# Optimization experiments

Hardware: AMD Instinct MI355X
Metric: run time of the kernel (lower is better)

## Reference

```python
import jax, jax.numpy as jnp
import numpy as np
import math

# Model dims (see init_kwargs)
B_SZ, L, D_MODEL = 1, 2048, 512
H, G, P, N, R = 16, 4, 64, 32, 2
RATIO = H // G
CHUNK = 256
EPS = 1e-5
DIM_Z = H * P
DIM_X = H * P
DIM_B = G * N * R
DIM_C = G * N * R
D_PROJ = DIM_Z + DIM_X + DIM_B + DIM_C + G + G


def setup_inputs() -> dict:
    key = jax.random.key(0)
    ks = jax.random.split(key, 8)
    u = jax.random.normal(ks[0], (B_SZ, L, D_MODEL), jnp.float32)
    W_in = jax.random.normal(ks[1], (D_PROJ, D_MODEL), jnp.float32) * (1.0 / math.sqrt(D_MODEL))
    b_in = np.zeros(D_PROJ, np.float32)
    # dt bias init: inverse softplus of dt ~ LogUniform(dt_min, dt_max)
    dt0 = np.exp(np.random.RandomState(0).rand(G) * (math.log(0.1) - math.log(0.001)) + math.log(0.001))
    inv_dt = dt0 + np.log(-np.expm1(-dt0))
    s = DIM_Z + DIM_X + DIM_B + DIM_C
    b_in[s:s + G] = inv_dt
    b_in[s + G:] = -3.0  # lambda bias
    b_in = jnp.asarray(b_in)
    W_xup = jax.random.normal(ks[2], (P * R, P), jnp.float32) * (1.0 / math.sqrt(P * R))
    W_ydown = jax.random.normal(ks[3], (P, P * R), jnp.float32) * (1.0 / math.sqrt(P * R))
    A_log = jnp.log(jax.random.uniform(ks[4], (G,), jnp.float32, 1.0, 16.0))
    theta_log = jax.random.normal(ks[5], (G, N // 2), jnp.float32)
    D = jnp.ones((H,), jnp.float32)
    norm_B_w = jnp.ones((N * R,), jnp.float32)
    norm_C_w = jnp.ones((N * R,), jnp.float32)
    bias_B = jnp.ones((G, N, R), jnp.float32)
    bias_C = jnp.ones((G, N, R), jnp.float32)
    W_out = jax.random.normal(ks[6], (D_MODEL, H * P), jnp.float32) * (1.0 / math.sqrt(H * P))
    return dict(u=u, W_in=W_in, b_in=b_in, W_xup=W_xup, W_ydown=W_ydown,
                A_log=A_log, theta_log=theta_log, D=D,
                norm_B_w=norm_B_w, norm_C_w=norm_C_w,
                bias_B=bias_B, bias_C=bias_C, W_out=W_out)


def _rms(x, w):
    return x * jax.lax.rsqrt(jnp.mean(x * x, axis=-1, keepdims=True) + EPS) * w


def _rope(x, ang):
    # x: (B,L,H,N,R), ang: (B,L,H,N/2) -- rotate interleaved (real,imag) pairs along N
    sh = x.shape
    xr = x.reshape(sh[:-2] + (N // 2, 2, R))
    re, im = xr[..., 0, :], xr[..., 1, :]
    c = jnp.cos(ang)[..., None]
    s = jnp.sin(ang)[..., None]
    out = jnp.stack([re * c - im * s, re * s + im * c], axis=-2)
    return out.reshape(sh)


def _chunk_scan(u, dt, A, C, cs):
    # u: (B,L,H,N,P), dt: (B,L,H), A: (H,), C: (B,L,H,N,R). L % cs == 0.
    B, Ltot, Hh, Nn, Pp = u.shape
    Rr = C.shape[-1]
    nc = Ltot // cs
    la = (dt * A).reshape(B, nc, cs, Hh)                      # log decay per step
    uc = u.reshape(B, nc, cs, Hh, Nn, Pp)
    Cc = C.reshape(B, nc, cs, Hh, Nn, Rr)
    # intra-chunk pairwise decay matrix (stable segsum)
    lap = la.transpose(0, 1, 3, 2)                            # (B,nc,H,cs)
    cums = jnp.cumsum(lap, axis=-1)
    seg = cums[..., :, None] - cums[..., None, :]
    mask = jnp.tril(jnp.ones((cs, cs), bool))
    Lmask = jnp.where(mask, jnp.exp(seg), 0.0)                # (B,nc,H,cs,cs)
    h_intra = jnp.einsum('bchij,bcjhnp->bcihnp', Lmask, uc)   # (B,nc,cs,H,N,P)
    y_diag = jnp.einsum('bclhnp,bclhnr->bclhpr', h_intra, Cc)
    decay_chunk = jnp.exp(jnp.sum(la, axis=2))                # (B,nc,H)
    h_last = h_intra[:, :, -1]                                # (B,nc,H,N,P)
    # inter-chunk sequential scan (state at the START of each chunk)
    def step(h, inp):
        d, cl = inp
        return h * d[:, :, None, None] + cl, h
    h0 = jnp.zeros((B, Hh, Nn, Pp), u.dtype)
    hF, h_states = jax.lax.scan(step, h0, (decay_chunk.transpose(1, 0, 2), h_last.transpose(1, 0, 2, 3, 4)))
    h_states = h_states.transpose(1, 0, 2, 3, 4)              # (B,nc,H,N,P)
    decay_intra = jnp.exp(jnp.cumsum(la, axis=2))             # (B,nc,cs,H)
    h_eff = jnp.einsum('bchnp,bclh->bclhnp', h_states, decay_intra)
    y_off = jnp.einsum('bclhnp,bclhnr->bclhpr', h_eff, Cc)
    y = (y_diag + y_off).reshape(B, Ltot, Hh, Pp, Rr)
    return y, hF


def reference(u, W_in, b_in, W_xup, W_ydown, A_log, theta_log, D,
              norm_B_w, norm_C_w, bias_B, bias_C, W_out):
    B_sz = u.shape[0]
    proj = u @ W_in.T + b_in                                  # (B,L,D_PROJ)
    s0, s1, s2, s3, s4 = DIM_Z, DIM_Z + DIM_X, DIM_Z + DIM_X + DIM_B, DIM_Z + DIM_X + DIM_B + DIM_C, DIM_Z + DIM_X + DIM_B + DIM_C + G
    z = proj[..., :s0]
    xp = proj[..., s0:s1].reshape(B_sz, L, H, P)
    Bp = proj[..., s1:s2]
    Cp = proj[..., s2:s3]
    dt = proj[..., s3:s4]                                     # (B,L,G)
    lam = proj[..., s4:]                                      # (B,L,G)
    xp = jax.nn.silu(xp)
    dt = jax.nn.softplus(dt)
    A = -jnp.exp(A_log)                                       # (G,)
    theta = jnp.exp(theta_log)                                # (G,N/2)
    # broadcast groups -> heads
    dt_h = jnp.repeat(dt, RATIO, axis=2)                      # (B,L,H)
    A_h = jnp.repeat(A, RATIO)                                # (H,)
    theta_h = jnp.repeat(theta, RATIO, axis=0)                # (H,N/2)
    lam_h = jax.nn.sigmoid(jnp.repeat(lam, RATIO, axis=2))    # (B,L,H)
    # data-dependent RoPE angles: cumulative dt*theta
    dt_theta = jnp.einsum('blh,hn->blhn', dt_h, theta_h)
    angles = jnp.cumsum(dt_theta, axis=1)                     # (B,L,H,N/2)
    # B / C: RMSNorm over N*R, add bias, broadcast groups, rotate
    Bp = _rms(Bp.reshape(B_sz, L, G, N * R), norm_B_w).reshape(B_sz, L, G, N, R) + bias_B
    Cp = _rms(Cp.reshape(B_sz, L, G, N * R), norm_C_w).reshape(B_sz, L, G, N, R) + bias_C
    B_rot = _rope(jnp.repeat(Bp, RATIO, axis=2), -angles)     # (B,L,H,N,R)
    C_rot = _rope(jnp.repeat(Cp, RATIO, axis=2), angles)
    # MIMO up projection
    x_up = (xp @ W_xup.T).reshape(B_sz, L, H, P, R)
    u_in = jnp.einsum('blhnr,blhpr->blhnp', B_rot, x_up) * dt_h[..., None, None]
    # generalized trapezoidal rule: mix current and decayed previous input
    alpha = jnp.exp(dt_h * A_h)                               # (B,L,H)
    u_prev = jnp.pad(u_in[:, :-1], ((0, 0), (1, 0), (0, 0), (0, 0), (0, 0)))
    u_eff = (1.0 - lam_h)[..., None, None] * u_in + (lam_h * alpha)[..., None, None] * u_prev
    y, _ = _chunk_scan(u_eff, dt_h, A_h, C_rot, CHUNK)        # (B,L,H,P,R)
    # MIMO down projection + D skip + gate
    y = y.reshape(B_sz, L, H, P * R) @ W_ydown.T              # (B,L,H,P)
    y = y + D[None, None, :, None] * xp
    y = y * jax.nn.silu(z.reshape(B_sz, L, H, P))
    out = y.reshape(B_sz, L, H * P) @ W_out.T
    return out
```

## Files before the change

### kernel.cpp

```cpp
#include <hip/hip_runtime.h>
#include <hip/hip_bf16.h>
#include <math.h>

namespace {

typedef unsigned short u16;
typedef __bf16 bf16x8 __attribute__((ext_vector_type(8)));
typedef float f32x4 __attribute__((ext_vector_type(4)));

constexpr int L_SEQ  = 2048;
constexpr int DPROJ  = 2568;
constexpr int OFF_X  = 1024;
constexpr int OFF_B  = 2048;
constexpr int OFF_C  = 2304;
constexpr int OFF_DT = 2560;
constexpr int SCHUNK = 16;
constexpr int NCH    = L_SEQ / SCHUNK;

__device__ inline u16 f2bf(float x) {
  unsigned u = __float_as_uint(x);
  unsigned r = u + 0x7FFFu + ((u >> 16) & 1u);
  return (u16)(r >> 16);
}
__device__ inline float bf2f(u16 h) {
  return __uint_as_float(((unsigned)h) << 16);
}

__device__ inline void split_body(const float* __restrict__ src, int rows,
                                  int cols, int stride, int idx,
                                  u16* __restrict__ hi, u16* __restrict__ lo)
{
  int c4cnt = cols >> 2;
  int row = idx / c4cnt;
  int c4  = (idx % c4cnt) << 2;
  float4 v = make_float4(0.f, 0.f, 0.f, 0.f);
  if (row < rows) v = *(const float4*)(src + (size_t)row * stride + c4);
  float x[4] = {v.x, v.y, v.z, v.w};
  u16 h[4], l[4];
#pragma unroll
  for (int j = 0; j < 4; ++j) {
    h[j] = f2bf(x[j]);
    l[j] = f2bf(x[j] - bf2f(h[j]));
  }
  size_t off = (size_t)row * cols + c4;
  *(ushort4*)(hi + off) = make_ushort4(h[0], h[1], h[2], h[3]);
  *(ushort4*)(lo + off) = make_ushort4(l[0], l[1], l[2], l[3]);
}

__global__ __launch_bounds__(256)
void convert_split(const float* __restrict__ src, int rows, int cols, int stride,
                   int rows_pad, u16* __restrict__ hi, u16* __restrict__ lo)
{
  int idx = blockIdx.x * 256 + threadIdx.x;
  if (idx >= rows_pad * (cols >> 2)) return;
  split_body(src, rows, cols, stride, idx, hi, lo);
}

__global__ __launch_bounds__(256)
void convert_weights(const float* __restrict__ W_in, const float* __restrict__ W_xup,
                     const float* __restrict__ W_ydown, const float* __restrict__ W_out,
                     u16* __restrict__ win_hi, u16* __restrict__ win_lo,
                     u16* __restrict__ wxup_hi, u16* __restrict__ wxup_lo,
                     u16* __restrict__ wyd_hi, u16* __restrict__ wyd_lo,
                     u16* __restrict__ wout_hi, u16* __restrict__ wout_lo)
{
  int b = blockIdx.x;
  if (b < 1344) {
    split_body(W_in, 2568, 512, 512, b * 256 + threadIdx.x, win_hi, win_lo);
  } else if (b < 1352) {
    split_body(W_xup, 128, 64, 64, (b - 1344) * 256 + threadIdx.x, wxup_hi, wxup_lo);
  } else if (b < 1360) {
    split_body(W_ydown, 64, 128, 128, (b - 1352) * 256 + threadIdx.x, wyd_hi, wyd_lo);
  } else {
    split_body(W_out, 512, 1024, 1024, (b - 1360) * 256 + threadIdx.x, wout_hi, wout_lo);
  }
}

__device__ inline void gload16(const u16* g, u16* l) {
  __builtin_amdgcn_global_load_lds(
      (const __attribute__((address_space(1))) unsigned int*)g,
      (__attribute__((address_space(3))) unsigned int*)l, 16, 0, 0);
}

__device__ inline void xcd_swizzle(int& bx, int& by, int& bz) {
  int nx = gridDim.x, ny = gridDim.y;
  int nwg = nx * ny * gridDim.z;
  int flat = blockIdx.x + nx * (blockIdx.y + ny * blockIdx.z);
  int cpx = nwg >> 3;
  int swz = (flat & 7) * cpx + (flat >> 3);
  bx = swz % nx;
  int r = swz / nx;
  by = r % ny;
  bz = r / ny;
}

template<int WMW, int WNW, bool GATE>
__global__ __launch_bounds__(64 * WMW * WNW)
void gemm_mfma(const u16* __restrict__ Ah, const u16* __restrict__ Al,
               const u16* __restrict__ Bh, const u16* __restrict__ Bl,
               const float* __restrict__ bias,
               float* __restrict__ C, int ldc, int N,
               int Kstride, int Klen, size_t c_slice,
               const float* __restrict__ Dv,
               const u16* __restrict__ xs_hi, const u16* __restrict__ xs_lo,
               const float* __restrict__ projz,
               u16* __restrict__ yg_hi, u16* __restrict__ yg_lo)
{
  constexpr int BM = 64 * WMW, BN = 64 * WNW;
  constexpr int WAVES = WMW * WNW;
  constexpr int RG_A = BM / 16, RG_B = BN / 16;
  constexpr int NG = 2 * RG_A + 2 * RG_B;
  constexpr int GPW = NG / WAVES;
  static_assert(NG % WAVES == 0, "");

  __shared__ u16 sAB[2][NG * 512];

  int bx, by, bz;
  xcd_swizzle(bx, by, bz);

  const int tid  = threadIdx.x;
  const int wave = tid >> 6;
  const int lane = tid & 63;
  const int wm   = wave % WMW;
  const int wn   = wave / WMW;
  const int bm   = bx * BM;
  const int bn   = by * BN;
  const int koff = bz * Klen;
  const int lrow = lane & 15;
  const int lkc  = lane >> 4;
  const int sr   = lane >> 2;
  const int sk8  = (lane & 3) * 8;

  const u16* gptr[GPW];
#pragma unroll
  for (int t = 0; t < GPW; ++t) {
    int g = wave * GPW + t;
    const u16* base;
    int rowbase;
    if (g < 2 * RG_A) {
      int hl = g / RG_A, i = g % RG_A;
      base = hl ? Al : Ah;  rowbase = bm + i * 16;
    } else {
      int g2 = g - 2 * RG_A;
      int hl = g2 / RG_B, i = g2 % RG_B;
      base = hl ? Bl : Bh;  rowbase = bn + i * 16;
    }
    gptr[t] = base + (size_t)(rowbase + sr) * Kstride + koff + sk8;
  }

  f32x4 acc[4][4];
#pragma unroll
  for (int i = 0; i < 4; ++i)
#pragma unroll
    for (int j = 0; j < 4; ++j) acc[i][j] = (f32x4){0.f, 0.f, 0.f, 0.f};

#define STAGE(b, kk)                                             \
  {                                                              \
    _Pragma("unroll")                                            \
    for (int t = 0; t < GPW; ++t)                                \
      gload16(gptr[t] + (kk), &sAB[b][(wave * GPW + t) * 512]);  \
  }

  STAGE(0, 0);
  asm volatile("s_waitcnt vmcnt(0)" ::: "memory");
  __syncthreads();

  int buf = 0;
  for (int k0 = 0; k0 < Klen; k0 += 32) {
    if (k0 + 32 < Klen) STAGE(buf ^ 1, k0 + 32);

    const u16* sb = sAB[buf];
    bf16x8 a_h[4], a_l[4], b_h[4], b_l[4];
#pragma unroll
    for (int i = 0; i < 4; ++i) {
      a_h[i] = *(const bf16x8*)&sb[(0 * RG_A + wm * 4 + i) * 512 + lrow * 32 + lkc * 8];
      a_l[i] = *(const bf16x8*)&sb[(1 * RG_A + wm * 4 + i) * 512 + lrow * 32 + lkc * 8];
      b_h[i] = *(const bf16x8*)&sb[(2 * RG_A + 0 * RG_B + wn * 4 + i) * 512 + lrow * 32 + lkc * 8];
      b_l[i] = *(const bf16x8*)&sb[(2 * RG_A + 1 * RG_B + wn * 4 + i) * 512 + lrow * 32 + lkc * 8];
    }
#pragma unroll
    for (int i = 0; i < 4; ++i)
#pragma unroll
      for (int j = 0; j < 4; ++j) {
        acc[i][j] = __builtin_amdgcn_mfma_f32_16x16x32_bf16(a_h[i], b_h[j], acc[i][j], 0, 0, 0);
        acc[i][j] = __builtin_amdgcn_mfma_f32_16x16x32_bf16(a_l[i], b_h[j], acc[i][j], 0, 0, 0);
        acc[i][j] = __builtin_amdgcn_mfma_f32_16x16x32_bf16(a_h[i], b_l[j], acc[i][j], 0, 0, 0);
      }

    asm volatile("s_waitcnt vmcnt(0)" ::: "memory");
    __syncthreads();
    buf ^= 1;
  }
#undef STAGE

  const int r0 = (lane >> 4) * 4;
  if (!GATE) {
    float* Cs = C + (size_t)bz * c_slice;
#pragma unroll
    for (int j = 0; j < 4; ++j) {
      int col = bn + wn * 64 + j * 16 + lrow;
      if (col >= N) continue;
      float bv = bias ? bias[col] : 0.f;
#pragma unroll
      for (int i = 0; i < 4; ++i) {
        int rowb = bm + wm * 64 + i * 16 + r0;
#pragma unroll
        for (int r = 0; r < 4; ++r)
          Cs[(size_t)(rowb + r) * ldc + col] = acc[i][j][r] + bv;
      }
    }
  } else {
#pragma unroll
    for (int j = 0; j < 4; ++j) {
      int col = bn + wn * 64 + j * 16 + lrow;
#pragma unroll
      for (int i = 0; i < 4; ++i) {
        int rowb = bm + wm * 64 + i * 16 + r0;
#pragma unroll
        for (int r = 0; r < 4; ++r) {
          int row = rowb + r;
          int l = row >> 4, h = row & 15;
          size_t ei = (size_t)l * 1024 + (h << 6) + col;
          float xsv = bf2f(xs_hi[ei]) + bf2f(xs_lo[ei]);
          float z = projz[(size_t)l * DPROJ + (h << 6) + col];
          float v = (acc[i][j][r] + Dv[h] * xsv) * (z / (1.f + expf(-z)));
          u16 hh = f2bf(v);
          yg_hi[ei] = hh;
          yg_lo[ei] = f2bf(v - bf2f(hh));
        }
      }
    }
  }
}

__global__ __launch_bounds__(256)
void reduce4_kernel(const float* __restrict__ p, float* __restrict__ o)
{
  const int n = L_SEQ * 512 / 4;
  int i = blockIdx.x * 256 + threadIdx.x;
  if (i >= n) return;
  float4 a = ((const float4*)p)[i];
  float4 b = ((const float4*)p)[i + n];
  float4 c = ((const float4*)p)[i + 2 * n];
  float4 d = ((const float4*)p)[i + 3 * n];
  float4 r;
  r.x = (a.x + b.x) + (c.x + d.x);
  r.y = (a.y + b.y) + (c.y + d.y);
  r.z = (a.z + b.z) + (c.z + d.z);
  r.w = (a.w + b.w) + (c.w + d.w);
  ((float4*)o)[i] = r;
}

__global__ __launch_bounds__(256)
void dtlam_kernel(const float* __restrict__ u, const float* __restrict__ W_in,
                  const float* __restrict__ b_in, const float* __restrict__ A_log,
                  float* __restrict__ dtg, float* __restrict__ alphag,
                  float* __restrict__ c0g, float* __restrict__ c1g)
{
  int idx = blockIdx.x * 256 + threadIdx.x;
  if (idx >= L_SEQ * 4) return;
  int l = idx >> 2, g = idx & 3;
  const float4* ur = (const float4*)(u + (size_t)l * 512);
  const float4* wd = (const float4*)(W_in + (size_t)(OFF_DT + g) * 512);
  const float4* wl = (const float4*)(W_in + (size_t)(OFF_DT + 4 + g) * 512);
  float sd = 0.f, sl = 0.f;
  for (int k = 0; k < 128; ++k) {
    float4 a = ur[k], b = wd[k], c = wl[k];
    sd += a.x * b.x + a.y * b.y + a.z * b.z + a.w * b.w;
    sl += a.x * c.x + a.y * c.y + a.z * c.z + a.w * c.w;
  }
  sd += b_in[OFF_DT + g];
  sl += b_in[OFF_DT + 4 + g];
  float dt  = (sd > 20.f) ? sd : log1pf(expf(sd));
  float lam = 1.f / (1.f + expf(-sl));
  float Ag  = -expf(A_log[g]);
  float al  = expf(dt * Ag);
  dtg[idx]    = dt;
  alphag[idx] = al;
  c0g[idx]    = 1.f - lam;
  c1g[idx]    = lam * al;
}

__global__ __launch_bounds__(256)
void cumsum_dt_kernel(const float* __restrict__ dtg, float* __restrict__ cumdt)
{
  const int g = blockIdx.x;
  const int t = threadIdx.x;
  constexpr int PER = L_SEQ / 256;
  __shared__ double ps[256];
  float loc[PER];
  double s = 0.0;
  int l0 = t * PER;
  for (int i = 0; i < PER; ++i) {
    loc[i] = dtg[(l0 + i) * 4 + g];
    s += (double)loc[i];
  }
  ps[t] = s;
  __syncthreads();
  for (int off = 1; off < 256; off <<= 1) {
    double v = (t >= off) ? ps[t - off] : 0.0;
    __syncthreads();
    ps[t] += v;
    __syncthreads();
  }
  double c = ps[t] - s;
  for (int i = 0; i < PER; ++i) {
    c += (double)loc[i];
    cumdt[(l0 + i) * 4 + g] = (float)c;
  }
}

__global__ __launch_bounds__(256)
void pertoken_kernel(const float* __restrict__ proj,
                     const float* __restrict__ cumdt,
                     const float* __restrict__ theta_log,
                     const float* __restrict__ norm_B_w,
                     const float* __restrict__ norm_C_w,
                     const float* __restrict__ bias_B,
                     const float* __restrict__ bias_C,
                     u16* __restrict__ xs_hi, u16* __restrict__ xs_lo,
                     float* __restrict__ Brot,
                     float* __restrict__ Crot)
{
  const int l = blockIdx.x;
  const int t = threadIdx.x;
  const size_t prow = (size_t)l * DPROJ;

  for (int i = t; i < 1024; i += 256) {
    float x = proj[prow + OFF_X + i];
    float s = x / (1.f + expf(-x));
    u16 hh = f2bf(s);
    xs_hi[(size_t)l * 1024 + i] = hh;
    xs_lo[(size_t)l * 1024 + i] = f2bf(s - bf2f(hh));
  }

  const int g = t >> 6;
  const int e = t & 63;
  float bv = proj[prow + OFF_B + t];
  float cv = proj[prow + OFF_C + t];
  float ssb = bv * bv, ssc = cv * cv;
#pragma unroll
  for (int m = 1; m <= 32; m <<= 1) {
    ssb += __shfl_xor(ssb, m, 64);
    ssc += __shfl_xor(ssc, m, 64);
  }
  float nb = bv * rsqrtf(ssb * (1.f / 64.f) + 1e-5f) * norm_B_w[e] + bias_B[t];
  float nc = cv * rsqrtf(ssc * (1.f / 64.f) + 1e-5f) * norm_C_w[e] + bias_C[t];

  float ang = expf(theta_log[g * 16 + (e >> 2)]) * cumdt[l * 4 + g];
  float ca, sa;
  sincosf(ang, &sa, &ca);
  float nb2 = __shfl_xor(nb, 2, 64);
  float nc2 = __shfl_xor(nc, 2, 64);
  bool isre = ((e >> 1) & 1) == 0;
  float Bo, Co;
  if (isre) {
    Bo = nb * ca + nb2 * sa;
    Co = nc * ca - nc2 * sa;
  } else {
    Bo = nb * ca - nb2 * sa;
    Co = nc * ca + nc2 * sa;
  }
  Brot[(size_t)l * 256 + t] = Bo;
  Crot[(size_t)l * 256 + t] = Co;
}

template<bool WITH_Y>
__global__ __launch_bounds__(256)
void scan_chunk(const float* __restrict__ Brot, const float* __restrict__ Crot,
                const float* __restrict__ xup,
                const float* __restrict__ dtg, const float* __restrict__ alphag,
                const float* __restrict__ c0g, const float* __restrict__ c1g,
                const float* __restrict__ hstates_in,
                float* __restrict__ hlast_out,
                u16* __restrict__ yhi, u16* __restrict__ ylo)
{
  const int c   = blockIdx.x;
  const int g   = blockIdx.y;
  const int wid = threadIdx.x >> 6;
  const int p   = threadIdx.x & 63;
  const int h   = g * 4 + wid;
  const int l0  = c * SCHUNK;

  __shared__ float Bs[SCHUNK][64];
  __shared__ float Cs[SCHUNK][64];
  __shared__ float als[SCHUNK], c0s[SCHUNK], c1s[SCHUNK];

  for (int i = threadIdx.x; i < SCHUNK * 64; i += 256) {
    int l = i >> 6, e = i & 63;
    float dt = dtg[(l0 + l) * 4 + g];
    Bs[l][e] = dt * Brot[(size_t)(l0 + l) * 256 + g * 64 + e];
    if (WITH_Y) Cs[l][e] = Crot[(size_t)(l0 + l) * 256 + g * 64 + e];
  }
  if (threadIdx.x < SCHUNK) {
    int l = threadIdx.x;
    als[l] = alphag[(l0 + l) * 4 + g];
    c0s[l] = c0g[(l0 + l) * 4 + g];
    c1s[l] = c1g[(l0 + l) * 4 + g];
  }
  __syncthreads();

  float H[32], up[32];
  if (WITH_Y) {
    const float* hs = &hstates_in[(((size_t)c * 16 + h) * 64 + p) * 32];
#pragma unroll
    for (int q = 0; q < 8; ++q) {
      float4 v = *reinterpret_cast<const float4*>(hs + 4 * q);
      H[4 * q] = v.x; H[4 * q + 1] = v.y; H[4 * q + 2] = v.z; H[4 * q + 3] = v.w;
    }
  } else {
#pragma unroll
    for (int n = 0; n < 32; ++n) H[n] = 0.f;
  }

  if (c > 0) {
    const int lm = l0 - 1;
    const float dtm = dtg[lm * 4 + g];
    float2 X = *reinterpret_cast<const float2*>(&xup[((size_t)lm * 16 + h) * 128 + 2 * p]);
    float x0 = dtm * X.x, x1 = dtm * X.y;
#pragma unroll
    for (int n = 0; n < 32; ++n) {
      float2 Bv = *reinterpret_cast<const float2*>(&Brot[(size_t)lm * 256 + g * 64 + 2 * n]);
      up[n] = Bv.x * x0 + Bv.y * x1;
    }
  } else {
#pragma unroll
    for (int n = 0; n < 32; ++n) up[n] = 0.f;
  }

  for (int l = 0; l < SCHUNK; ++l) {
    float2 X = *reinterpret_cast<const float2*>(
        &xup[((size_t)(l0 + l) * 16 + h) * 128 + 2 * p]);
    const float al = als[l], cc0 = c0s[l], cc1 = c1s[l];
    float y0 = 0.f, y1 = 0.f;
#pragma unroll
    for (int n2 = 0; n2 < 16; ++n2) {
      float4 Bv = *reinterpret_cast<const float4*>(&Bs[l][4 * n2]);
      float uin0 = Bv.x * X.x + Bv.y * X.y;
      float uin1 = Bv.z * X.x + Bv.w * X.y;
      float ue0 = cc0 * uin0 + cc1 * up[2 * n2];
      float ue1 = cc0 * uin1 + cc1 * up[2 * n2 + 1];
      H[2 * n2]     = al * H[2 * n2]     + ue0;
      H[2 * n2 + 1] = al * H[2 * n2 + 1] + ue1;
      up[2 * n2] = uin0; up[2 * n2 + 1] = uin1;
      if (WITH_Y) {
        float4 Cv = *reinterpret_cast<const float4*>(&Cs[l][4 * n2]);
        y0 = fmaf(H[2 * n2], Cv.x, fmaf(H[2 * n2 + 1], Cv.z, y0));
        y1 = fmaf(H[2 * n2], Cv.y, fmaf(H[2 * n2 + 1], Cv.w, y1));
      }
    }
    if (WITH_Y) {
      size_t ofs = ((size_t)(l0 + l) * 16 + h) * 128 + 2 * p;
      u16 h0 = f2bf(y0), h1 = f2bf(y1);
      *(ushort2*)&yhi[ofs] = make_ushort2(h0, h1);
      *(ushort2*)&ylo[ofs] = make_ushort2(f2bf(y0 - bf2f(h0)), f2bf(y1 - bf2f(h1)));
    }
  }

  if (!WITH_Y) {
    float* hl = &hlast_out[(((size_t)c * 16 + h) * 64 + p) * 32];
#pragma unroll
    for (int q = 0; q < 8; ++q)
      *reinterpret_cast<float4*>(hl + 4 * q) =
          make_float4(H[4 * q], H[4 * q + 1], H[4 * q + 2], H[4 * q + 3]);
  }
}

__global__ __launch_bounds__(256)
void scan_passB(const float* __restrict__ hlast, const float* __restrict__ cumdt,
                const float* __restrict__ A_log, float* __restrict__ hstates)
{
  int idx = blockIdx.x * 256 + threadIdx.x;
  int h = idx >> 11;
  int rem = idx & 2047;
  int g = h >> 2;
  float Ag = -expf(A_log[g]);
  float s = 0.f;
  for (int c0 = 0; c0 < NCH; c0 += 8) {
    float hlv[8], dec[8];
#pragma unroll
    for (int j = 0; j < 8; ++j) {
      int c = c0 + j;
      hlv[j] = hlast[((size_t)c * 16 + h) * 2048 + rem];
      float sd = cumdt[(c * SCHUNK + SCHUNK - 1) * 4 + g]
               - (c > 0 ? cumdt[(c * SCHUNK - 1) * 4 + g] : 0.f);
      dec[j] = expf(Ag * sd);
    }
#pragma unroll
    for (int j = 0; j < 8; ++j) {
      hstates[((size_t)(c0 + j) * 16 + h) * 2048 + rem] = s;
      s = fmaf(s, dec[j], hlv[j]);
    }
  }
}

}

extern "C" void kernel_launch(void* const* d_in, const int* in_sizes, int n_in,
                              void* d_out, int out_size, void* d_ws, size_t ws_size,
                              hipStream_t stream)
{
  const float* u         = (const float*)d_in[0];
  const float* W_in      = (const float*)d_in[1];
  const float* b_in      = (const float*)d_in[2];
  const float* W_xup     = (const float*)d_in[3];
  const float* W_ydown   = (const float*)d_in[4];
  const float* A_log     = (const float*)d_in[5];
  const float* theta_log = (const float*)d_in[6];
  const float* Dvec      = (const float*)d_in[7];
  const float* norm_B_w  = (const float*)d_in[8];
  const float* norm_C_w  = (const float*)d_in[9];
  const float* bias_B    = (const float*)d_in[10];
  const float* bias_C    = (const float*)d_in[11];
  const float* W_out     = (const float*)d_in[12];
  float* out = (float*)d_out;

  float* proj    = (float*)d_ws;
  float* xsreg   = proj    + (size_t)L_SEQ * DPROJ;
  float* dtg     = xsreg   + (size_t)L_SEQ * 1024;
  float* alphag  = dtg     + L_SEQ * 4;
  float* c0g     = alphag  + L_SEQ * 4;
  float* c1g     = c0g     + L_SEQ * 4;
  float* cumdt   = c1g     + L_SEQ * 4;
  float* Brot    = cumdt   + L_SEQ * 4;
  float* Crot    = Brot    + (size_t)L_SEQ * 256;
  float* xup     = Crot    + (size_t)L_SEQ * 256;
  float* y128s   = xup     + (size_t)32768 * 128;
  float* rAf     = y128s   + (size_t)32768 * 128;
  float* hlast   = rAf     + (size_t)5100000;
  float* hstates = hlast   + (size_t)NCH * 16 * 2048;
  float* partials = y128s;

  u16* xs_hi = (u16*)xsreg;
  u16* xs_lo = xs_hi + (size_t)L_SEQ * 1024;
  u16* y128_hi = (u16*)y128s;
  u16* y128_lo = y128_hi + (size_t)32768 * 128;

  u16* rA = (u16*)rAf;
  u16* win_hi  = rA;
  u16* win_lo  = win_hi  + (size_t)2688 * 512;
  u16* wxup_hi = win_lo  + (size_t)2688 * 512;
  u16* wxup_lo = wxup_hi + (size_t)128 * 64;
  u16* wyd_hi  = wxup_lo + (size_t)128 * 64;
  u16* wyd_lo  = wyd_hi  + (size_t)64 * 128;
  u16* wout_hi = wyd_lo  + (size_t)64 * 128;
  u16* wout_lo = wout_hi + (size_t)512 * 1024;
  u16* u_hi    = wout_lo + (size_t)512 * 1024;
  u16* u_lo    = u_hi    + (size_t)2048 * 512;
  u16* yg_hi   = u_lo    + (size_t)2048 * 512;
  u16* yg_lo   = yg_hi   + (size_t)2048 * 1024;

  convert_weights<<<dim3(1872), 256, 0, stream>>>(
      W_in, W_xup, W_ydown, W_out,
      win_hi, win_lo, wxup_hi, wxup_lo, wyd_hi, wyd_lo, wout_hi, wout_lo);
  convert_split<<<dim3(1024), 256, 0, stream>>>(u, 2048, 512, 512, 2048, u_hi, u_lo);
  gemm_mfma<2, 2, false><<<dim3(16, 21, 1), 256, 0, stream>>>(
      u_hi, u_lo, win_hi, win_lo, b_in, proj, DPROJ, DPROJ, 512, 512, 0,
      nullptr, nullptr, nullptr, nullptr, nullptr, nullptr);

  dtlam_kernel<<<dim3(32), 256, 0, stream>>>(u, W_in, b_in, A_log, dtg, alphag, c0g, c1g);
  cumsum_dt_kernel<<<dim3(4), 256, 0, stream>>>(dtg, cumdt);

  pertoken_kernel<<<dim3(L_SEQ), 256, 0, stream>>>(
      proj, cumdt, theta_log, norm_B_w, norm_C_w, bias_B, bias_C,
      xs_hi, xs_lo, Brot, Crot);

  gemm_mfma<2, 2, false><<<dim3(256, 1, 1), 256, 0, stream>>>(
      xs_hi, xs_lo, wxup_hi, wxup_lo, nullptr, xup, 128, 128, 64, 64, 0,
      nullptr, nullptr, nullptr, nullptr, nullptr, nullptr);

  scan_chunk<false><<<dim3(NCH, 4), 256, 0, stream>>>(
      Brot, Crot, xup, dtg, alphag, c0g, c1g, nullptr, hlast, nullptr, nullptr);
  scan_passB<<<dim3(128), 256, 0, stream>>>(hlast, cumdt, A_log, hstates);
  scan_chunk<true><<<dim3(NCH, 4), 256, 0, stream>>>(
      Brot, Crot, xup, dtg, alphag, c0g, c1g, hstates, nullptr, y128_hi, y128_lo);

  gemm_mfma<2, 1, true><<<dim3(256, 1, 1), 128, 0, stream>>>(
      y128_hi, y128_lo, wyd_hi, wyd_lo, nullptr, nullptr, 0, 64, 128, 128, 0,
      Dvec, xs_hi, xs_lo, proj, yg_hi, yg_lo);

  gemm_mfma<2, 2, false><<<dim3(16, 4, 4), 256, 0, stream>>>(
      yg_hi, yg_lo, wout_hi, wout_lo, nullptr, partials, 512, 512, 1024, 256,
      (size_t)L_SEQ * 512,
      nullptr, nullptr, nullptr, nullptr, nullptr, nullptr);
  reduce4_kernel<<<dim3(1024), 256, 0, stream>>>(partials, out);
}
```

Measured before the change: 189.0 us.

## Merge input conversion kernels, parallelize dt dot products, precompute reduced RoPE angles

Folds the u split conversion into the weight conversion kernel, saving one launch. Splits each dt/lambda dot product across 16 lanes with a shuffle reduction, so 512 blocks run instead of 32 serial 512-long loops. The cumsum kernel now computes the RoPE angles in double precision, reduces them modulo 2π and stores them, so pertoken only loads the angle. This mainly improves accuracy, but it adds serial double-precision work and extra writes to the 4-block cumsum kernel.

```diff
diff --git a/kernel.cpp b/kernel.cpp
--- a/kernel.cpp
+++ b/kernel.cpp
@@ -48,21 +48,14 @@
 }
 
 __global__ __launch_bounds__(256)
-void convert_split(const float* __restrict__ src, int rows, int cols, int stride,
-                   int rows_pad, u16* __restrict__ hi, u16* __restrict__ lo)
-{
-  int idx = blockIdx.x * 256 + threadIdx.x;
-  if (idx >= rows_pad * (cols >> 2)) return;
-  split_body(src, rows, cols, stride, idx, hi, lo);
-}
-
-__global__ __launch_bounds__(256)
-void convert_weights(const float* __restrict__ W_in, const float* __restrict__ W_xup,
-                     const float* __restrict__ W_ydown, const float* __restrict__ W_out,
-                     u16* __restrict__ win_hi, u16* __restrict__ win_lo,
-                     u16* __restrict__ wxup_hi, u16* __restrict__ wxup_lo,
-                     u16* __restrict__ wyd_hi, u16* __restrict__ wyd_lo,
-                     u16* __restrict__ wout_hi, u16* __restrict__ wout_lo)
+void convert_all(const float* __restrict__ W_in, const float* __restrict__ W_xup,
+                 const float* __restrict__ W_ydown, const float* __restrict__ W_out,
+                 const float* __restrict__ u,
+                 u16* __restrict__ win_hi, u16* __restrict__ win_lo,
+                 u16* __restrict__ wxup_hi, u16* __restrict__ wxup_lo,
+                 u16* __restrict__ wyd_hi, u16* __restrict__ wyd_lo,
+                 u16* __restrict__ wout_hi, u16* __restrict__ wout_lo,
+                 u16* __restrict__ u_hi, u16* __restrict__ u_lo)
 {
   int b = blockIdx.x;
   if (b < 1344) {
@@ -71,8 +64,10 @@
     split_body(W_xup, 128, 64, 64, (b - 1344) * 256 + threadIdx.x, wxup_hi, wxup_lo);
   } else if (b < 1360) {
     split_body(W_ydown, 64, 128, 128, (b - 1352) * 256 + threadIdx.x, wyd_hi, wyd_lo);
+  } else if (b < 1872) {
+    split_body(W_out, 512, 1024, 1024, (b - 1360) * 256 + threadIdx.x, wout_hi, wout_lo);
   } else {
-    split_body(W_out, 512, 1024, 1024, (b - 1360) * 256 + threadIdx.x, wout_hi, wout_lo);
+    split_body(u, 2048, 512, 512, (b - 1872) * 256 + threadIdx.x, u_hi, u_lo);
   }
 }
 
@@ -257,37 +252,51 @@
                   float* __restrict__ dtg, float* __restrict__ alphag,
                   float* __restrict__ c0g, float* __restrict__ c1g)
 {
-  int idx = blockIdx.x * 256 + threadIdx.x;
-  if (idx >= L_SEQ * 4) return;
-  int l = idx >> 2, g = idx & 3;
-  const float4* ur = (const float4*)(u + (size_t)l * 512);
-  const float4* wd = (const float4*)(W_in + (size_t)(OFF_DT + g) * 512);
-  const float4* wl = (const float4*)(W_in + (size_t)(OFF_DT + 4 + g) * 512);
+  int tid  = blockIdx.x * 256 + threadIdx.x;
+  int pair = tid >> 4;
+  int ln   = tid & 15;
+  int l = pair >> 2, g = pair & 3;
+  const float4* ur = (const float4*)(u + (size_t)l * 512) + ln * 8;
+  const float4* wd = (const float4*)(W_in + (size_t)(OFF_DT + g) * 512) + ln * 8;
+  const float4* wl = (const float4*)(W_in + (size_t)(OFF_DT + 4 + g) * 512) + ln * 8;
   float sd = 0.f, sl = 0.f;
-  for (int k = 0; k < 128; ++k) {
+#pragma unroll
+  for (int k = 0; k < 8; ++k) {
     float4 a = ur[k], b = wd[k], c = wl[k];
     sd += a.x * b.x + a.y * b.y + a.z * b.z + a.w * b.w;
     sl += a.x * c.x + a.y * c.y + a.z * c.z + a.w * c.w;
   }
-  sd += b_in[OFF_DT + g];
-  sl += b_in[OFF_DT + 4 + g];
-  float dt  = (sd > 20.f) ? sd : log1pf(expf(sd));
-  float lam = 1.f / (1.f + expf(-sl));
-  float Ag  = -expf(A_log[g]);
-  float al  = expf(dt * Ag);
-  dtg[idx]    = dt;
-  alphag[idx] = al;
-  c0g[idx]    = 1.f - lam;
-  c1g[idx]    = lam * al;
+#pragma unroll
+  for (int m = 1; m < 16; m <<= 1) {
+    sd += __shfl_xor(sd, m, 64);
+    sl += __shfl_xor(sl, m, 64);
+  }
+  if (ln == 0) {
+    sd += b_in[OFF_DT + g];
+    sl += b_in[OFF_DT + 4 + g];
+    float dt  = (sd > 20.f) ? sd : log1pf(expf(sd));
+    float lam = 1.f / (1.f + expf(-sl));
+    float Ag  = -expf(A_log[g]);
+    float al  = expf(dt * Ag);
+    dtg[pair]    = dt;
+    alphag[pair] = al;
+    c0g[pair]    = 1.f - lam;
+    c1g[pair]    = lam * al;
+  }
 }
 
 __global__ __launch_bounds__(256)
-void cumsum_dt_kernel(const float* __restrict__ dtg, float* __restrict__ cumdt)
+void cumsum_dt_kernel(const float* __restrict__ dtg,
+                      const float* __restrict__ theta_log,
+                      float* __restrict__ cumdt, float* __restrict__ angred)
 {
   const int g = blockIdx.x;
   const int t = threadIdx.x;
   constexpr int PER = L_SEQ / 256;
   __shared__ double ps[256];
+  double th[16];
+#pragma unroll
+  for (int f = 0; f < 16; ++f) th[f] = exp((double)theta_log[g * 16 + f]);
   float loc[PER];
   double s = 0.0;
   int l0 = t * PER;
@@ -304,16 +313,23 @@
     __syncthreads();
   }
   double c = ps[t] - s;
+  const double inv2pi = 0.15915494309189535;
+  const double twopi  = 6.283185307179586;
   for (int i = 0; i < PER; ++i) {
     c += (double)loc[i];
     cumdt[(l0 + i) * 4 + g] = (float)c;
+#pragma unroll
+    for (int f = 0; f < 16; ++f) {
+      double rev = th[f] * c * inv2pi;
+      double fr  = rev - floor(rev);
+      angred[(size_t)(l0 + i) * 64 + g * 16 + f] = (float)(fr * twopi);
+    }
   }
 }
 
 __global__ __launch_bounds__(256)
 void pertoken_kernel(const float* __restrict__ proj,
-                     const float* __restrict__ cumdt,
-                     const float* __restrict__ theta_log,
+                     const float* __restrict__ angred,
                      const float* __restrict__ norm_B_w,
                      const float* __restrict__ norm_C_w,
                      const float* __restrict__ bias_B,
@@ -347,7 +363,7 @@
   float nb = bv * rsqrtf(ssb * (1.f / 64.f) + 1e-5f) * norm_B_w[e] + bias_B[t];
   float nc = cv * rsqrtf(ssc * (1.f / 64.f) + 1e-5f) * norm_C_w[e] + bias_C[t];
 
-  float ang = expf(theta_log[g * 16 + (e >> 2)]) * cumdt[l * 4 + g];
+  float ang = angred[(size_t)l * 64 + g * 16 + (e >> 2)];
   float ca, sa;
   sincosf(ang, &sa, &ca);
   float nb2 = __shfl_xor(nb, 2, 64);
@@ -522,7 +538,8 @@
   float* c0g     = alphag  + L_SEQ * 4;
   float* c1g     = c0g     + L_SEQ * 4;
   float* cumdt   = c1g     + L_SEQ * 4;
-  float* Brot    = cumdt   + L_SEQ * 4;
+  float* angred  = cumdt   + L_SEQ * 4;
+  float* Brot    = angred  + (size_t)L_SEQ * 64;
   float* Crot    = Brot    + (size_t)L_SEQ * 256;
   float* xup     = Crot    + (size_t)L_SEQ * 256;
   float* y128s   = xup     + (size_t)32768 * 128;
@@ -550,19 +567,19 @@
   u16* yg_hi   = u_lo    + (size_t)2048 * 512;
   u16* yg_lo   = yg_hi   + (size_t)2048 * 1024;
 
-  convert_weights<<<dim3(1872), 256, 0, stream>>>(
-      W_in, W_xup, W_ydown, W_out,
-      win_hi, win_lo, wxup_hi, wxup_lo, wyd_hi, wyd_lo, wout_hi, wout_lo);
-  convert_split<<<dim3(1024), 256, 0, stream>>>(u, 2048, 512, 512, 2048, u_hi, u_lo);
+  convert_all<<<dim3(2896), 256, 0, stream>>>(
+      W_in, W_xup, W_ydown, W_out, u,
+      win_hi, win_lo, wxup_hi, wxup_lo, wyd_hi, wyd_lo, wout_hi, wout_lo,
+      u_hi, u_lo);
   gemm_mfma<2, 2, false><<<dim3(16, 21, 1), 256, 0, stream>>>(
       u_hi, u_lo, win_hi, win_lo, b_in, proj, DPROJ, DPROJ, 512, 512, 0,
       nullptr, nullptr, nullptr, nullptr, nullptr, nullptr);
 
-  dtlam_kernel<<<dim3(32), 256, 0, stream>>>(u, W_in, b_in, A_log, dtg, alphag, c0g, c1g);
-  cumsum_dt_kernel<<<dim3(4), 256, 0, stream>>>(dtg, cumdt);
+  dtlam_kernel<<<dim3(512), 256, 0, stream>>>(u, W_in, b_in, A_log, dtg, alphag, c0g, c1g);
+  cumsum_dt_kernel<<<dim3(4), 256, 0, stream>>>(dtg, theta_log, cumdt, angred);
 
   pertoken_kernel<<<dim3(L_SEQ), 256, 0, stream>>>(
-      proj, cumdt, theta_log, norm_B_w, norm_C_w, bias_B, bias_C,
+      proj, angred, norm_B_w, norm_C_w, bias_B, bias_C,
       xs_hi, xs_lo, Brot, Crot);
 
   gemm_mfma<2, 2, false><<<dim3(256, 1, 1), 256, 0, stream>>>(
```

Result: faster. 162.6 us (-14.0%).
